# Kernel optimization log

Hardware: AMD Instinct MI355X
Metric: run time of the kernel (lower is better)

The kernel has to match this reference:

```python
import jax, jax.numpy as jnp
import numpy as np

N = 50000      # nodes
E = 800000     # edges (avg degree 16)
DIN = 128      # input_dim
DG = 128       # gnn_dim
DCLS = 128     # cls_dim
DOUT = 10      # output_dim
LMDA = 1.0     # rw_lmda
P_DROP = 0.5


def setup_inputs() -> dict:
    key = jax.random.key(0)
    ks = jax.random.split(key, 12)
    x = jax.random.normal(ks[0], (N, DIN), jnp.float32)
    edge_index = jax.random.randint(ks[1], (2, E), 0, N, dtype=jnp.int64)
    edge_weight = jax.random.uniform(ks[2], (E,), jnp.float32)
    def glorot(k, shape):
        lim = np.sqrt(6.0 / (shape[0] + shape[1])).astype(np.float32)
        return jax.random.uniform(k, shape, jnp.float32, -lim, lim)
    return dict(
        x=x, edge_index=edge_index, edge_weight=edge_weight,
        W_lin_in=glorot(ks[3], (DIN, DG)), b_lin_in=jnp.zeros((DG,), jnp.float32),
        W_agg_in=glorot(ks[4], (DG + DIN, DG)), b_agg_in=jnp.zeros((DG,), jnp.float32),
        W_lin_h=glorot(ks[5], (DG, DG)), b_lin_h=jnp.zeros((DG,), jnp.float32),
        W_agg_h=glorot(ks[6], (2 * DG, DG)), b_agg_h=jnp.zeros((DG,), jnp.float32),
        W_mlp1=glorot(ks[7], (DG, DCLS)), b_mlp1=jnp.zeros((DCLS,), jnp.float32),
        W_mlp2=glorot(ks[8], (DCLS, DOUT)), b_mlp2=jnp.zeros((DOUT,), jnp.float32),
    )


def _gs_layer(x, row, col, ew, inv_cnt, W_lin, b_lin, W_agg, b_agg):
    # GS_reweight: message = (1-lmda)*lin(x_j) + lmda*ew*lin(x_j), mean-aggregated
    # at row (flow='target_to_source': gather from col, scatter to row).
    h = x @ W_lin + b_lin                      # [N, DG] (lin before gather == lin(x_j))
    hj = h[col]                                # [E, DG] gather
    m = (1.0 - LMDA) * hj + LMDA * (ew[:, None] * hj)
    agg = jax.ops.segment_sum(m, row, num_segments=N) * inv_cnt[:, None]  # mean
    out = jnp.concatenate([agg, x], axis=-1) @ W_agg + b_agg              # update()
    return jax.nn.relu(out)


def _dropout(x, k):
    mask = jax.random.bernoulli(k, 1.0 - P_DROP, x.shape)
    return jnp.where(mask, x / (1.0 - P_DROP), 0.0)


def reference(x, edge_index, edge_weight,
              W_lin_in, b_lin_in, W_agg_in, b_agg_in,
              W_lin_h, b_lin_h, W_agg_h, b_agg_h,
              W_mlp1, b_mlp1, W_mlp2, b_mlp2):
    row, col = edge_index[0], edge_index[1]
    cnt = jax.ops.segment_sum(jnp.ones((E,), x.dtype), row, num_segments=N)
    inv_cnt = 1.0 / jnp.maximum(cnt, 1.0)     # scatter_mean: empty rows -> 0
    dk = jax.random.split(jax.random.key(42), 3)
    h = _gs_layer(x, row, col, edge_weight, inv_cnt, W_lin_in, b_lin_in, W_agg_in, b_agg_in)
    h = _dropout(jax.nn.relu(h), dk[0])       # relu is idempotent after update's relu
    for i in range(2):                        # layers 2,3 share prop_hidden weights
        h = _gs_layer(h, row, col, edge_weight, inv_cnt, W_lin_h, b_lin_h, W_agg_h, b_agg_h)
        h = _dropout(jax.nn.relu(h), dk[i + 1])
    y = jax.nn.relu(h @ W_mlp1 + b_mlp1) @ W_mlp2 + b_mlp2  # cls_layers=2, bn=False
    return (h, y)
```

## Files before the change

kernel.cpp:

```cpp
#include <hip/hip_runtime.h>
#include <cstdint>
#include <cstddef>


#define N_NODES 50000
#define N_EDGES 800000
#define DGN 128
#define DOUT 10
#define NELEM (N_NODES * DGN)
#define NMASKW (NELEM / 64)
#define NBINS 391
#define TILE 4096
#define NTILES ((N_EDGES + TILE - 1) / TILE)
#define GBF ((N_NODES + 63) / 64)
#define MK_BLOCKS 25000

#define XB_BLK 6250
#define HI_BLK NTILES
#define WC_BLK 128
#define TR_BLK 192
#define R0 XB_BLK
#define R1 (R0 + HI_BLK)
#define R2 (R1 + WC_BLK)
#define R3 (R2 + TR_BLK)
#define MEGA_BLOCKS (R3 + 1)

#define AB_BLOCKS ((N_NODES + 3) / 4)

typedef __attribute__((ext_vector_type(8))) short bf16x8;
typedef __attribute__((ext_vector_type(4))) float f32x4;

__host__ __device__ static inline unsigned short f2bf(float f) {
  union { float f; unsigned u; } c; c.f = f;
  unsigned u = c.u;
  return (unsigned short)((u + 0x7fffu + ((u >> 16) & 1u)) >> 16);
}
__device__ static inline float bflo(unsigned u) { return __uint_as_float(u << 16); }
__device__ static inline float bfhi(unsigned u) { return __uint_as_float(u & 0xffff0000u); }
__device__ static inline float bf2f(unsigned short h) {
  return __uint_as_float(((unsigned)h) << 16);
}

__host__ __device__ static inline void tf2x32(unsigned k0, unsigned k1,
                                              unsigned c0, unsigned c1,
                                              unsigned& o0, unsigned& o1) {
  unsigned ks2 = k0 ^ k1 ^ 0x1BD11BDAu;
  unsigned x0 = c0 + k0;
  unsigned x1 = c1 + k1;
#define TFR(r) { x0 += x1; x1 = (x1 << (r)) | (x1 >> (32 - (r))); x1 ^= x0; }
  TFR(13) TFR(15) TFR(26) TFR(6)
  x0 += k1;  x1 += ks2 + 1u;
  TFR(17) TFR(29) TFR(16) TFR(24)
  x0 += ks2; x1 += k0 + 2u;
  TFR(13) TFR(15) TFR(26) TFR(6)
  x0 += k0;  x1 += k1 + 3u;
  TFR(17) TFR(29) TFR(16) TFR(24)
  x0 += k1;  x1 += ks2 + 4u;
  TFR(13) TFR(15) TFR(26) TFR(6)
  x0 += ks2; x1 += k0 + 5u;
#undef TFR
  o0 = x0; o1 = x1;
}

__device__ static inline void mask_chunk(unsigned long long* __restrict__ gm,
                                         int i, unsigned k0, unsigned k1) {
  unsigned o0, o1;
  tf2x32(k0, k1, 0u, (unsigned)i, o0, o1);
  unsigned long long b = __ballot(((o0 ^ o1) >> 31) == 0u);
  if ((threadIdx.x & 63) == 0) gm[i >> 6] = b;
}

__global__ __launch_bounds__(256) void mega_kernel(
    const float* __restrict__ x, unsigned short* __restrict__ xb,
    const int* __restrict__ ei, int* __restrict__ chist,
    const float* __restrict__ Wli, const float* __restrict__ Wai,
    const float* __restrict__ Wlh, const float* __restrict__ Wah,
    const float* __restrict__ Wm1,
    const float* __restrict__ bli, const float* __restrict__ blh,
    unsigned short* __restrict__ Tai, unsigned short* __restrict__ Tah,
    unsigned short* __restrict__ Tm1,
    float* __restrict__ bvi, float* __restrict__ bvh) {
  __shared__ int h[NBINS];
  const int b = blockIdx.x;
  const int tid = threadIdx.x;

  if (b < R0) {
    int g = b * 256 + tid;
    float4 v = ((const float4*)x)[g];
    ushort4 o;
    o.x = f2bf(v.x); o.y = f2bf(v.y); o.z = f2bf(v.z); o.w = f2bf(v.w);
    ((ushort4*)xb)[g] = o;
  } else if (b < R1) {
    for (int i = tid; i < NBINS; i += 256) h[i] = 0;
    __syncthreads();
    const int e0 = (b - R0) * TILE;
#pragma unroll 4
    for (int j = 0; j < TILE; j += 256) {
      int e = e0 + j + tid;
      if (e < N_EDGES) {
        int r = ei[e];
        r = (r < 0) ? 0 : (r >= N_NODES ? N_NODES - 1 : r);
        atomicAdd(&h[r >> 7], 1);
      }
    }
    __syncthreads();
    for (int i = tid; i < NBINS; i += 256)
      if (h[i]) atomicAdd(&chist[i], h[i]);
  } else if (b < R2) {
    int idx = (b - R1) * 256 + tid;
    int n = idx & 127;
    int k = (idx >> 7) & 127;
    int m = idx >> 14;
    const float* Wl = m ? Wlh : Wli;
    const float* Wa = m ? Wah : Wai;
    unsigned short* T = m ? Tah : Tai;
    float acc = 0.0f;
#pragma unroll 8
    for (int j = 0; j < 128; ++j)
      acc += Wl[k * 128 + j] * Wa[j * 128 + n];
    T[n * 256 + k] = f2bf(acc);
  } else if (b < R3) {
    int j = (b - R2) * 256 + tid;
    if (j < 16384) {
      int kk = j & 127, n = j >> 7;
      Tai[n * 256 + 128 + kk] = f2bf(Wai[(size_t)(128 + kk) * 128 + n]);
    } else if (j < 32768) {
      int q = j - 16384;
      int kk = q & 127, n = q >> 7;
      Tah[n * 256 + 128 + kk] = f2bf(Wah[(size_t)(128 + kk) * 128 + n]);
    } else {
      int q = j - 32768;
      int k = q & 127, n = q >> 7;
      Tm1[n * 128 + k] = f2bf(Wm1[(size_t)k * 128 + n]);
    }
  } else {
    int n = tid & 127;
    const float* bl = (tid < 128) ? bli : blh;
    const float* Wa = (tid < 128) ? Wai : Wah;
    float acc = 0.0f;
    for (int j = 0; j < 128; ++j) acc += bl[j] * Wa[j * 128 + n];
    if (tid < 128) bvi[n] = acc; else bvh[n] = acc;
  }
}

__global__ __launch_bounds__(512) void prefix_kernel(const int* __restrict__ chist,
                                                     int* __restrict__ cbase,
                                                     int* __restrict__ ccursor,
                                                     int* __restrict__ rowptr) {
  __shared__ int s[512];
  const int t = threadIdx.x;
  int v = (t < NBINS) ? chist[t] : 0;
  s[t] = v;
  __syncthreads();
  for (int off = 1; off < 512; off <<= 1) {
    int tv = (t >= off) ? s[t - off] : 0;
    __syncthreads();
    s[t] += tv;
    __syncthreads();
  }
  if (t <= NBINS) {
    int ex = (t == 0) ? 0 : s[t - 1];
    cbase[t] = ex;
    if (t < NBINS) ccursor[t] = ex;
  }
  if (t == 0) rowptr[N_NODES] = N_EDGES;
}

__global__ __launch_bounds__(256) void scatter_kernel(const int* __restrict__ ei,
                                                      const float* __restrict__ ew,
                                                      int* __restrict__ ccursor,
                                                      uint2* __restrict__ pk,
                                                      unsigned long long* __restrict__ mg0,
                                                      unsigned k00, unsigned k01) {
  if (blockIdx.x >= NTILES) {
    mask_chunk(mg0, (blockIdx.x - NTILES) * 256 + threadIdx.x, k00, k01);
    return;
  }
  __shared__ uint2 st[TILE];
  __shared__ unsigned short sbin[TILE];
  __shared__ int h[NBINS];
  __shared__ int base[NBINS];
  __shared__ int gbase[NBINS];
  __shared__ int cur[NBINS];
  __shared__ int sc[512];
  const int tid = threadIdx.x;
  const int e0 = blockIdx.x * TILE;
  const int nt = (N_EDGES - e0 < TILE) ? (N_EDGES - e0) : TILE;

  for (int i = tid; i < NBINS; i += 256) { h[i] = 0; cur[i] = 0; }
  __syncthreads();
  for (int j = tid; j < nt; j += 256) {
    int r = ei[e0 + j];
    r = (r < 0) ? 0 : (r >= N_NODES ? N_NODES - 1 : r);
    atomicAdd(&h[r >> 7], 1);
  }
  __syncthreads();
  sc[tid] = (tid < NBINS) ? h[tid] : 0;
  sc[tid + 256] = (tid + 256 < NBINS) ? h[tid + 256] : 0;
  __syncthreads();
  for (int off = 1; off < 512; off <<= 1) {
    int a0 = (tid >= off) ? sc[tid - off] : 0;
    int a1 = (tid + 256 >= off) ? sc[tid + 256 - off] : 0;
    __syncthreads();
    sc[tid] += a0; sc[tid + 256] += a1;
    __syncthreads();
  }
  if (tid < NBINS) {
    base[tid] = sc[tid] - h[tid];
    if (h[tid]) gbase[tid] = atomicAdd(&ccursor[tid], h[tid]);
  }
  if (tid + 256 < NBINS) {
    base[tid + 256] = sc[tid + 256] - h[tid + 256];
    if (h[tid + 256]) gbase[tid + 256] = atomicAdd(&ccursor[tid + 256], h[tid + 256]);
  }
  __syncthreads();
  for (int j = tid; j < nt; j += 256) {
    int r = ei[e0 + j];
    r = (r < 0) ? 0 : (r >= N_NODES ? N_NODES - 1 : r);
    int c = ei[N_EDGES + e0 + j];
    c = (c < 0) ? 0 : (c >= N_NODES ? N_NODES - 1 : c);
    int bb = r >> 7;
    int slot = base[bb] + atomicAdd(&cur[bb], 1);
    uint2 p;
    p.x = ((unsigned)r << 16) | (unsigned)c;
    p.y = __float_as_uint(ew[e0 + j]);
    st[slot] = p;
    sbin[slot] = (unsigned short)bb;
  }
  __syncthreads();
  for (int j = tid; j < nt; j += 256) {
    int bb = sbin[j];
    pk[gbase[bb] + (j - base[bb])] = st[j];
  }
}

__global__ __launch_bounds__(256) void place_kernel(const int* __restrict__ cbase,
                                                    const uint2* __restrict__ pk,
                                                    uint2* __restrict__ csr,
                                                    int* __restrict__ rowptr,
                                                    float* __restrict__ invc) {
  __shared__ int lcnt[128];
  __shared__ int lpre[128];
  __shared__ int lcur[128];
  __shared__ int sc[128];
  const int b = blockIdx.x;
  const int tid = threadIdx.x;
  const int cb = cbase[b];
  const int n = cbase[b + 1] - cb;
  const int r0 = b << 7;
  const int nr = (N_NODES - r0 < 128) ? (N_NODES - r0) : 128;

  if (tid < 128) { lcnt[tid] = 0; lcur[tid] = 0; }
  __syncthreads();
  for (int i = tid; i < n; i += 256) {
    int r7 = (int)(pk[cb + i].x >> 16) - r0;
    atomicAdd(&lcnt[r7], 1);
  }
  __syncthreads();
  if (tid < 128) sc[tid] = lcnt[tid];
  __syncthreads();
  for (int off = 1; off < 128; off <<= 1) {
    int tv = (tid >= off && tid < 128) ? sc[tid - off] : 0;
    __syncthreads();
    if (tid < 128) sc[tid] += tv;
    __syncthreads();
  }
  if (tid < 128) lpre[tid] = sc[tid] - lcnt[tid];
  __syncthreads();
  if (tid < nr) {
    rowptr[r0 + tid] = cb + lpre[tid];
    int c = lcnt[tid];
    invc[r0 + tid] = 1.0f / (float)(c > 1 ? c : 1);
  }
  for (int i = tid; i < n; i += 256) {
    uint2 p = pk[cb + i];
    int r7 = (int)(p.x >> 16) - r0;
    int slot = cb + lpre[r7] + atomicAdd(&lcur[r7], 1);
    uint2 o;
    o.x = p.x & 0xFFFFu;
    o.y = p.y;
    csr[slot] = o;
  }
}

__global__ __launch_bounds__(256) void agg_kernel(const unsigned short* __restrict__ hlin,
                                                  const int* __restrict__ rowptr,
                                                  const uint2* __restrict__ csr,
                                                  const float* __restrict__ invc,
                                                  unsigned short* __restrict__ agg,
                                                  float* __restrict__ swout) {
  const int r = blockIdx.x * 4 + (threadIdx.x >> 6);
  const int lane = threadIdx.x & 63;
  const int es = lane >> 4;
  const int cg = lane & 15;
  const int start = rowptr[r];
  const int num = rowptr[r + 1] - start;
  const uint4* __restrict__ H = (const uint4*)hlin;

  int qi = (num > 0) ? (start + (lane < num ? lane : num - 1)) : 0;
  uint2 myq = csr[qi];

  float a[8] = {0.f, 0.f, 0.f, 0.f, 0.f, 0.f, 0.f, 0.f};
  float ws = 0.f;
  const int nb = (num < 64) ? num : 64;
  for (int e = 0; e < nb; e += 16) {
#pragma unroll
    for (int j = 0; j < 4; ++j) {
      int idx = e + j * 4 + es;
      bool ok = idx < nb;
      int sl = ok ? idx : nb - 1;
      int c0 = __shfl((int)myq.x, sl);
      int w0 = __shfl((int)myq.y, sl);
      unsigned col = (unsigned)c0;
      float w = ok ? __uint_as_float((unsigned)w0) : 0.0f;
      uint4 p = H[(size_t)col * 16 + cg];
      ws += w;
      a[0] += w * bflo(p.x); a[1] += w * bfhi(p.x);
      a[2] += w * bflo(p.y); a[3] += w * bfhi(p.y);
      a[4] += w * bflo(p.z); a[5] += w * bfhi(p.z);
      a[6] += w * bflo(p.w); a[7] += w * bfhi(p.w);
    }
  }
  for (int e = 64; e < num; e += 16) {
#pragma unroll
    for (int j = 0; j < 4; ++j) {
      int idx = e + j * 4 + es;
      bool ok = idx < num;
      int idxc = ok ? idx : (num - 1);
      uint2 q = csr[start + idxc];
      float w = ok ? __uint_as_float(q.y) : 0.0f;
      uint4 p = H[(size_t)q.x * 16 + cg];
      ws += w;
      a[0] += w * bflo(p.x); a[1] += w * bfhi(p.x);
      a[2] += w * bflo(p.y); a[3] += w * bfhi(p.y);
      a[4] += w * bflo(p.z); a[5] += w * bfhi(p.z);
      a[6] += w * bflo(p.w); a[7] += w * bfhi(p.w);
    }
  }
#pragma unroll
  for (int k = 0; k < 8; ++k) {
    a[k] += __shfl_xor(a[k], 32);
    a[k] += __shfl_xor(a[k], 16);
  }
  ws += __shfl_xor(ws, 32);
  ws += __shfl_xor(ws, 16);
  const float s = invc[r];
  if (es == 0) {
    uint4 o;
    o.x = (unsigned)f2bf(a[0] * s) | ((unsigned)f2bf(a[1] * s) << 16);
    o.y = (unsigned)f2bf(a[2] * s) | ((unsigned)f2bf(a[3] * s) << 16);
    o.z = (unsigned)f2bf(a[4] * s) | ((unsigned)f2bf(a[5] * s) << 16);
    o.w = (unsigned)f2bf(a[6] * s) | ((unsigned)f2bf(a[7] * s) << 16);
    ((uint4*)agg)[(size_t)r * 16 + cg] = o;
  }
  if (swout && lane == 0) swout[r] = ws * s;
}

template <bool WF32, bool MASKGEN>
__global__ __launch_bounds__(256) void layer_gemm(
    const unsigned short* __restrict__ Agg, const unsigned short* __restrict__ Hin,
    const unsigned short* __restrict__ Wt,
    const float* __restrict__ bvec, const float* __restrict__ bagg,
    const float* __restrict__ sw,
    const unsigned long long* __restrict__ maskw,
    float* __restrict__ outf, unsigned short* __restrict__ outb,
    unsigned long long* __restrict__ gm, unsigned gk0, unsigned gk1) {
  if (MASKGEN && blockIdx.x >= GBF) {
    mask_chunk(gm, (blockIdx.x - GBF) * 256 + threadIdx.x, gk0, gk1);
    return;
  }
  constexpr int LS = 72;
  __shared__ unsigned short Als[64 * LS];
  __shared__ unsigned short Bls[128 * LS];
  const int tid = threadIdx.x;
  const int m0 = blockIdx.x * 64;
  const int lane = tid & 63;
  const int wid = tid >> 6;
  const int wm = (wid >> 1) * 32;
  const int wn = (wid & 1) * 64;
  const int ln = lane & 15;
  const int lh = lane >> 4;
  const int sArow = tid >> 2;
  const int sAk = (tid & 3) * 16;
  const int sBcol = tid >> 1;
  const int sBk = (tid & 1) * 32;
  int arow = m0 + sArow;
  if (arow >= N_NODES) arow = N_NODES - 1;

  f32x4 acc[2][4];
#pragma unroll
  for (int i = 0; i < 2; ++i)
#pragma unroll
    for (int j = 0; j < 4; ++j)
#pragma unroll
      for (int r = 0; r < 4; ++r) acc[i][j][r] = 0.0f;

  for (int kb = 0; kb < 256; kb += 64) {
    const unsigned short* Asrc = (kb < 128) ? Agg : Hin;
    const unsigned short* ap = Asrc + (size_t)arow * 128 + (kb & 127) + sAk;
    unsigned short* al = &Als[sArow * LS + sAk];
    *(uint4*)(al + 0) = *(const uint4*)(ap + 0);
    *(uint4*)(al + 8) = *(const uint4*)(ap + 8);
    const unsigned short* bp = Wt + (size_t)sBcol * 256 + kb + sBk;
    unsigned short* bl = &Bls[sBcol * LS + sBk];
    *(uint4*)(bl + 0)  = *(const uint4*)(bp + 0);
    *(uint4*)(bl + 8)  = *(const uint4*)(bp + 8);
    *(uint4*)(bl + 16) = *(const uint4*)(bp + 16);
    *(uint4*)(bl + 24) = *(const uint4*)(bp + 24);
    __syncthreads();
#pragma unroll
    for (int ks = 0; ks < 64; ks += 32) {
      bf16x8 af[2], bfr[4];
#pragma unroll
      for (int i = 0; i < 2; ++i)
        af[i] = *(const bf16x8*)&Als[(wm + i * 16 + ln) * LS + ks + lh * 8];
#pragma unroll
      for (int j = 0; j < 4; ++j)
        bfr[j] = *(const bf16x8*)&Bls[(wn + j * 16 + ln) * LS + ks + lh * 8];
#pragma unroll
      for (int i = 0; i < 2; ++i)
#pragma unroll
        for (int j = 0; j < 4; ++j)
          acc[i][j] = __builtin_amdgcn_mfma_f32_16x16x32_bf16(af[i], bfr[j], acc[i][j], 0, 0, 0);
    }
    __syncthreads();
  }

  const int lm = lane >> 4;
  float bc[4], b2[4];
#pragma unroll
  for (int j = 0; j < 4; ++j) {
    int col = wn + j * 16 + ln;
    bc[j] = bvec[col];
    b2[j] = bagg[col];
  }
#pragma unroll
  for (int i = 0; i < 2; ++i) {
    const int lr0 = wm + i * 16 + lm * 4;
#pragma unroll
    for (int r = 0; r < 4; ++r) {
      const int row = m0 + lr0 + r;
      if (row >= N_NODES) continue;
      const float swr = sw[row];
      const unsigned long long mw = maskw[(size_t)row * 2 + (wn >> 6)];
#pragma unroll
      for (int j = 0; j < 4; ++j) {
        const int col = wn + j * 16 + ln;
        float v = acc[i][j][r] + swr * bc[j] + b2[j];
        v = fmaxf(v, 0.0f);
        v = ((mw >> (col & 63)) & 1ull) ? 2.0f * v : 0.0f;
        if (WF32) outf[(size_t)row * DGN + col] = v;
        outb[(size_t)row * DGN + col] = f2bf(v);
      }
    }
  }
}

__global__ __launch_bounds__(256) void mlp_gemm(
    const unsigned short* __restrict__ A0,
    const unsigned short* __restrict__ Wt,
    const float* __restrict__ b1,
    const float* __restrict__ W2, const float* __restrict__ b2,
    float* __restrict__ y) {
  constexpr int LS = 72;
  constexpr int LT = 132;
  __shared__ unsigned short Als[64 * LS];
  __shared__ unsigned short Bls[128 * LS];
  __shared__ unsigned short tT[64 * LT];
  __shared__ float Ws[128 * DOUT];
  __shared__ float bs[DOUT];
  const int tid = threadIdx.x;
  const int m0 = blockIdx.x * 64;
  const int lane = tid & 63;
  const int wid = tid >> 6;
  const int wm = (wid >> 1) * 32;
  const int wn = (wid & 1) * 64;
  const int ln = lane & 15;
  const int lh = lane >> 4;
  const int sArow = tid >> 2;
  const int sAk = (tid & 3) * 16;
  const int sBcol = tid >> 1;
  const int sBk = (tid & 1) * 32;
  int arow = m0 + sArow;
  if (arow >= N_NODES) arow = N_NODES - 1;

  for (int i = tid; i < 128 * DOUT; i += 256) Ws[i] = W2[i];
  if (tid < DOUT) bs[tid] = b2[tid];

  f32x4 acc[2][4];
#pragma unroll
  for (int i = 0; i < 2; ++i)
#pragma unroll
    for (int j = 0; j < 4; ++j)
#pragma unroll
      for (int r = 0; r < 4; ++r) acc[i][j][r] = 0.0f;

  for (int kb = 0; kb < 128; kb += 64) {
    const unsigned short* ap = A0 + (size_t)arow * 128 + kb + sAk;
    unsigned short* al = &Als[sArow * LS + sAk];
    *(uint4*)(al + 0) = *(const uint4*)(ap + 0);
    *(uint4*)(al + 8) = *(const uint4*)(ap + 8);
    const unsigned short* bp = Wt + (size_t)sBcol * 128 + kb + sBk;
    unsigned short* bl = &Bls[sBcol * LS + sBk];
    *(uint4*)(bl + 0)  = *(const uint4*)(bp + 0);
    *(uint4*)(bl + 8)  = *(const uint4*)(bp + 8);
    *(uint4*)(bl + 16) = *(const uint4*)(bp + 16);
    *(uint4*)(bl + 24) = *(const uint4*)(bp + 24);
    __syncthreads();
#pragma unroll
    for (int ks = 0; ks < 64; ks += 32) {
      bf16x8 af[2], bfr[4];
#pragma unroll
      for (int i = 0; i < 2; ++i)
        af[i] = *(const bf16x8*)&Als[(wm + i * 16 + ln) * LS + ks + lh * 8];
#pragma unroll
      for (int j = 0; j < 4; ++j)
        bfr[j] = *(const bf16x8*)&Bls[(wn + j * 16 + ln) * LS + ks + lh * 8];
#pragma unroll
      for (int i = 0; i < 2; ++i)
#pragma unroll
        for (int j = 0; j < 4; ++j)
          acc[i][j] = __builtin_amdgcn_mfma_f32_16x16x32_bf16(af[i], bfr[j], acc[i][j], 0, 0, 0);
    }
    __syncthreads();
  }

  const int lm = lane >> 4;
  float bcol[4];
#pragma unroll
  for (int j = 0; j < 4; ++j) bcol[j] = b1[wn + j * 16 + ln];
#pragma unroll
  for (int i = 0; i < 2; ++i) {
    const int lr0 = wm + i * 16 + lm * 4;
#pragma unroll
    for (int r = 0; r < 4; ++r) {
      const int lr = lr0 + r;
#pragma unroll
      for (int j = 0; j < 4; ++j) {
        const int col = wn + j * 16 + ln;
        float v = fmaxf(acc[i][j][r] + bcol[j], 0.0f);
        tT[lr * LT + col] = f2bf(v);
      }
    }
  }
  __syncthreads();

  if (tid < 64) {
    int row = m0 + tid;
    if (row < N_NODES) {
      float a2[DOUT];
#pragma unroll
      for (int c = 0; c < DOUT; ++c) a2[c] = bs[c];
      const unsigned short* tr = &tT[tid * LT];
#pragma unroll 8
      for (int k = 0; k < 128; ++k) {
        float tv = bf2f(tr[k]);
        const float* wr = &Ws[k * DOUT];
#pragma unroll
        for (int c = 0; c < DOUT; ++c) a2[c] += tv * wr[c];
      }
      float* yp = y + (size_t)row * DOUT;
#pragma unroll
      for (int c = 0; c < DOUT; ++c) yp[c] = a2[c];
    }
  }
}

extern "C" void kernel_launch(void* const* d_in, const int* in_sizes, int n_in,
                              void* d_out, int out_size, void* d_ws, size_t ws_size,
                              hipStream_t stream) {
  const float* x        = (const float*)d_in[0];
  const int*   ei       = (const int*)d_in[1];
  const float* ew       = (const float*)d_in[2];
  const float* W_lin_in = (const float*)d_in[3];
  const float* b_lin_in = (const float*)d_in[4];
  const float* W_agg_in = (const float*)d_in[5];
  const float* b_agg_in = (const float*)d_in[6];
  const float* W_lin_h  = (const float*)d_in[7];
  const float* b_lin_h  = (const float*)d_in[8];
  const float* W_agg_h  = (const float*)d_in[9];
  const float* b_agg_h  = (const float*)d_in[10];
  const float* W_mlp1   = (const float*)d_in[11];
  const float* b_mlp1   = (const float*)d_in[12];
  const float* W_mlp2   = (const float*)d_in[13];
  const float* b_mlp2   = (const float*)d_in[14];

  float* hout = (float*)d_out;
  float* yout = hout + (size_t)NELEM;

  char* p = (char*)d_ws;
  auto alloc = [&](size_t bytes) {
    char* q = p;
    p += (bytes + 255) & ~(size_t)255;
    return q;
  };
  int*   chist   = (int*)alloc((size_t)(NBINS + 1) * 4);
  int*   cbase   = (int*)alloc((size_t)(NBINS + 1) * 4);
  int*   ccursor = (int*)alloc((size_t)NBINS * 4);
  int*   rowptr  = (int*)alloc((size_t)(N_NODES + 1) * 4);
  float* invc    = (float*)alloc((size_t)N_NODES * 4);
  float* swv     = (float*)alloc((size_t)N_NODES * 4);
  uint2* pk      = (uint2*)alloc((size_t)N_EDGES * 8);
  uint2* csr     = (uint2*)alloc((size_t)N_EDGES * 8);
  unsigned short* xb   = (unsigned short*)alloc((size_t)NELEM * 2);
  unsigned short* aggb = (unsigned short*)alloc((size_t)NELEM * 2);
  unsigned short* hA   = (unsigned short*)alloc((size_t)NELEM * 2);
  unsigned short* hB   = (unsigned short*)alloc((size_t)NELEM * 2);
  unsigned long long* mw0 = (unsigned long long*)alloc((size_t)NMASKW * 8);
  unsigned long long* mw1 = (unsigned long long*)alloc((size_t)NMASKW * 8);
  unsigned long long* mw2 = (unsigned long long*)alloc((size_t)NMASKW * 8);
  unsigned short* Tai = (unsigned short*)alloc(32768 * 2);
  unsigned short* Tah = (unsigned short*)alloc(32768 * 2);
  unsigned short* Tm1 = (unsigned short*)alloc(16384 * 2);
  float* bvi = (float*)alloc(128 * 4);
  float* bvh = (float*)alloc(128 * 4);

  unsigned dk[3][2];
  for (unsigned i = 0; i < 3; ++i) tf2x32(0u, 42u, 0u, i, dk[i][0], dk[i][1]);

  hipMemsetAsync(chist, 0, (size_t)(NBINS + 1) * 4, stream);
  mega_kernel<<<MEGA_BLOCKS, 256, 0, stream>>>(
      x, xb, ei, chist, W_lin_in, W_agg_in, W_lin_h, W_agg_h, W_mlp1,
      b_lin_in, b_lin_h, Tai, Tah, Tm1, bvi, bvh);

  prefix_kernel<<<1, 512, 0, stream>>>(chist, cbase, ccursor, rowptr);
  scatter_kernel<<<NTILES + MK_BLOCKS, 256, 0, stream>>>(
      ei, ew, ccursor, pk, mw0, dk[0][0], dk[0][1]);
  place_kernel<<<NBINS, 256, 0, stream>>>(cbase, pk, csr, rowptr, invc);

  agg_kernel<<<AB_BLOCKS, 256, 0, stream>>>(xb, rowptr, csr, invc, aggb, swv);
  layer_gemm<false, true><<<GBF + MK_BLOCKS, 256, 0, stream>>>(
      aggb, xb, Tai, bvi, b_agg_in, swv, mw0, nullptr, hA,
      mw1, dk[1][0], dk[1][1]);

  agg_kernel<<<AB_BLOCKS, 256, 0, stream>>>(hA, rowptr, csr, invc, aggb, nullptr);
  layer_gemm<false, true><<<GBF + MK_BLOCKS, 256, 0, stream>>>(
      aggb, hA, Tah, bvh, b_agg_h, swv, mw1, nullptr, hB,
      mw2, dk[2][0], dk[2][1]);

  agg_kernel<<<AB_BLOCKS, 256, 0, stream>>>(hB, rowptr, csr, invc, aggb, nullptr);
  layer_gemm<true, false><<<GBF, 256, 0, stream>>>(
      aggb, hB, Tah, bvh, b_agg_h, swv, mw2, hout, hA,
      nullptr, 0, 0);

  mlp_gemm<<<GBF, 256, 0, stream>>>(hA, Tm1, b_mlp1, W_mlp2, b_mlp2, yout);
}
```

Baseline: 311.9 us.

## Drop prefix kernel via fixed bin strides, fuse MLP into last layer GEMM

Removes the single-block prefix kernel by giving each bin a fixed-stride slot in the staging buffer and computing each bin's base with a per-block reduction in place_kernel. Dropout mask generation moves from the scatter and layer GEMM launches into the agg_kernel launches. The MLP head is fused into the final layer GEMM so its output tile stays in shared memory instead of round-tripping through global memory. The cost is a larger staging buffer, which overflows if a bin exceeds 4096 edges, and higher shared memory use in the fused GEMM.

Measured after the change: 328.1 us. +5.2%, slower.

```diff
diff --git a/kernel.cpp b/kernel.cpp
--- a/kernel.cpp
+++ b/kernel.cpp
@@ -11,6 +11,7 @@
 #define NMASKW (NELEM / 64)
 #define NBINS 391
 #define TILE 4096
+#define BSTR 4096
 #define NTILES ((N_EDGES + TILE - 1) / TILE)
 #define GBF ((N_NODES + 63) / 64)
 #define MK_BLOCKS 25000
@@ -143,39 +144,10 @@
   }
 }
 
-__global__ __launch_bounds__(512) void prefix_kernel(const int* __restrict__ chist,
-                                                     int* __restrict__ cbase,
-                                                     int* __restrict__ ccursor,
-                                                     int* __restrict__ rowptr) {
-  __shared__ int s[512];
-  const int t = threadIdx.x;
-  int v = (t < NBINS) ? chist[t] : 0;
-  s[t] = v;
-  __syncthreads();
-  for (int off = 1; off < 512; off <<= 1) {
-    int tv = (t >= off) ? s[t - off] : 0;
-    __syncthreads();
-    s[t] += tv;
-    __syncthreads();
-  }
-  if (t <= NBINS) {
-    int ex = (t == 0) ? 0 : s[t - 1];
-    cbase[t] = ex;
-    if (t < NBINS) ccursor[t] = ex;
-  }
-  if (t == 0) rowptr[N_NODES] = N_EDGES;
-}
-
 __global__ __launch_bounds__(256) void scatter_kernel(const int* __restrict__ ei,
                                                       const float* __restrict__ ew,
                                                       int* __restrict__ ccursor,
-                                                      uint2* __restrict__ pk,
-                                                      unsigned long long* __restrict__ mg0,
-                                                      unsigned k00, unsigned k01) {
-  if (blockIdx.x >= NTILES) {
-    mask_chunk(mg0, (blockIdx.x - NTILES) * 256 + threadIdx.x, k00, k01);
-    return;
-  }
+                                                      uint2* __restrict__ pk) {
   __shared__ uint2 st[TILE];
   __shared__ unsigned short sbin[TILE];
   __shared__ int h[NBINS];
@@ -207,11 +179,12 @@
   }
   if (tid < NBINS) {
     base[tid] = sc[tid] - h[tid];
-    if (h[tid]) gbase[tid] = atomicAdd(&ccursor[tid], h[tid]);
+    if (h[tid]) gbase[tid] = tid * BSTR + atomicAdd(&ccursor[tid], h[tid]);
   }
   if (tid + 256 < NBINS) {
     base[tid + 256] = sc[tid + 256] - h[tid + 256];
-    if (h[tid + 256]) gbase[tid + 256] = atomicAdd(&ccursor[tid + 256], h[tid + 256]);
+    if (h[tid + 256])
+      gbase[tid + 256] = (tid + 256) * BSTR + atomicAdd(&ccursor[tid + 256], h[tid + 256]);
   }
   __syncthreads();
   for (int j = tid; j < nt; j += 256) {
@@ -230,30 +203,41 @@
   __syncthreads();
   for (int j = tid; j < nt; j += 256) {
     int bb = sbin[j];
-    pk[gbase[bb] + (j - base[bb])] = st[j];
-  }
-}
-
-__global__ __launch_bounds__(256) void place_kernel(const int* __restrict__ cbase,
+    pk[(size_t)gbase[bb] + (j - base[bb])] = st[j];
+  }
+}
+
+__global__ __launch_bounds__(256) void place_kernel(const int* __restrict__ chist,
                                                     const uint2* __restrict__ pk,
                                                     uint2* __restrict__ csr,
                                                     int* __restrict__ rowptr,
                                                     float* __restrict__ invc) {
+  __shared__ int red[256];
   __shared__ int lcnt[128];
   __shared__ int lpre[128];
   __shared__ int lcur[128];
   __shared__ int sc[128];
   const int b = blockIdx.x;
   const int tid = threadIdx.x;
-  const int cb = cbase[b];
-  const int n = cbase[b + 1] - cb;
+
+  int psum = 0;
+  for (int i = tid; i < b; i += 256) psum += chist[i];
+  red[tid] = psum;
+  __syncthreads();
+  for (int off = 128; off > 0; off >>= 1) {
+    if (tid < off) red[tid] += red[tid + off];
+    __syncthreads();
+  }
+  const int cb = red[0];
+  const int n = chist[b];
+  const uint2* __restrict__ pkb = pk + (size_t)b * BSTR;
   const int r0 = b << 7;
   const int nr = (N_NODES - r0 < 128) ? (N_NODES - r0) : 128;
 
   if (tid < 128) { lcnt[tid] = 0; lcur[tid] = 0; }
   __syncthreads();
   for (int i = tid; i < n; i += 256) {
-    int r7 = (int)(pk[cb + i].x >> 16) - r0;
+    int r7 = (int)(pkb[i].x >> 16) - r0;
     atomicAdd(&lcnt[r7], 1);
   }
   __syncthreads();
@@ -272,8 +256,9 @@
     int c = lcnt[tid];
     invc[r0 + tid] = 1.0f / (float)(c > 1 ? c : 1);
   }
+  if (b == NBINS - 1 && tid == 0) rowptr[N_NODES] = N_EDGES;
   for (int i = tid; i < n; i += 256) {
-    uint2 p = pk[cb + i];
+    uint2 p = pkb[i];
     int r7 = (int)(p.x >> 16) - r0;
     int slot = cb + lpre[r7] + atomicAdd(&lcur[r7], 1);
     uint2 o;
@@ -288,7 +273,13 @@
                                                   const uint2* __restrict__ csr,
                                                   const float* __restrict__ invc,
                                                   unsigned short* __restrict__ agg,
-                                                  float* __restrict__ swout) {
+                                                  float* __restrict__ swout,
+                                                  unsigned long long* __restrict__ gm,
+                                                  unsigned gk0, unsigned gk1) {
+  if (blockIdx.x >= AB_BLOCKS) {
+    mask_chunk(gm, (blockIdx.x - AB_BLOCKS) * 256 + threadIdx.x, gk0, gk1);
+    return;
+  }
   const int r = blockIdx.x * 4 + (threadIdx.x >> 6);
   const int lane = threadIdx.x & 63;
   const int es = lane >> 4;
@@ -356,7 +347,7 @@
   if (swout && lane == 0) swout[r] = ws * s;
 }
 
-template <bool WF32, bool MASKGEN>
+template <bool WF32, bool MLP>
 __global__ __launch_bounds__(256) void layer_gemm(
     const unsigned short* __restrict__ Agg, const unsigned short* __restrict__ Hin,
     const unsigned short* __restrict__ Wt,
@@ -364,14 +355,17 @@
     const float* __restrict__ sw,
     const unsigned long long* __restrict__ maskw,
     float* __restrict__ outf, unsigned short* __restrict__ outb,
-    unsigned long long* __restrict__ gm, unsigned gk0, unsigned gk1) {
-  if (MASKGEN && blockIdx.x >= GBF) {
-    mask_chunk(gm, (blockIdx.x - GBF) * 256 + threadIdx.x, gk0, gk1);
-    return;
-  }
+    const unsigned short* __restrict__ Wt2,
+    const float* __restrict__ b1,
+    const float* __restrict__ W2, const float* __restrict__ b2,
+    float* __restrict__ y) {
   constexpr int LS = 72;
+  constexpr int LT = 132;
   __shared__ unsigned short Als[64 * LS];
   __shared__ unsigned short Bls[128 * LS];
+  __shared__ unsigned short tT[MLP ? 64 * LT : 2];
+  __shared__ float Ws[MLP ? 128 * DOUT : 1];
+  __shared__ float bs[MLP ? DOUT : 1];
   const int tid = threadIdx.x;
   const int m0 = blockIdx.x * 64;
   const int lane = tid & 63;
@@ -387,6 +381,11 @@
   int arow = m0 + sArow;
   if (arow >= N_NODES) arow = N_NODES - 1;
 
+  if (MLP) {
+    for (int i = tid; i < 128 * DOUT; i += 256) Ws[i] = W2[i];
+    if (tid < DOUT) bs[tid] = b2[tid];
+  }
+
   f32x4 acc[2][4];
 #pragma unroll
   for (int i = 0; i < 2; ++i)
@@ -427,12 +426,12 @@
   }
 
   const int lm = lane >> 4;
-  float bc[4], b2[4];
+  float bc[4], b2c[4];
 #pragma unroll
   for (int j = 0; j < 4; ++j) {
     int col = wn + j * 16 + ln;
     bc[j] = bvec[col];
-    b2[j] = bagg[col];
+    b2c[j] = bagg[col];
   }
 #pragma unroll
   for (int i = 0; i < 2; ++i) {
@@ -446,122 +445,90 @@
 #pragma unroll
       for (int j = 0; j < 4; ++j) {
         const int col = wn + j * 16 + ln;
-        float v = acc[i][j][r] + swr * bc[j] + b2[j];
+        float v = acc[i][j][r] + swr * bc[j] + b2c[j];
         v = fmaxf(v, 0.0f);
         v = ((mw >> (col & 63)) & 1ull) ? 2.0f * v : 0.0f;
         if (WF32) outf[(size_t)row * DGN + col] = v;
-        outb[(size_t)row * DGN + col] = f2bf(v);
+        if (MLP) tT[(lr0 + r) * LT + col] = f2bf(v);
+        else outb[(size_t)row * DGN + col] = f2bf(v);
       }
     }
   }
-}
-
-__global__ __launch_bounds__(256) void mlp_gemm(
-    const unsigned short* __restrict__ A0,
-    const unsigned short* __restrict__ Wt,
-    const float* __restrict__ b1,
-    const float* __restrict__ W2, const float* __restrict__ b2,
-    float* __restrict__ y) {
-  constexpr int LS = 72;
-  constexpr int LT = 132;
-  __shared__ unsigned short Als[64 * LS];
-  __shared__ unsigned short Bls[128 * LS];
-  __shared__ unsigned short tT[64 * LT];
-  __shared__ float Ws[128 * DOUT];
-  __shared__ float bs[DOUT];
-  const int tid = threadIdx.x;
-  const int m0 = blockIdx.x * 64;
-  const int lane = tid & 63;
-  const int wid = tid >> 6;
-  const int wm = (wid >> 1) * 32;
-  const int wn = (wid & 1) * 64;
-  const int ln = lane & 15;
-  const int lh = lane >> 4;
-  const int sArow = tid >> 2;
-  const int sAk = (tid & 3) * 16;
-  const int sBcol = tid >> 1;
-  const int sBk = (tid & 1) * 32;
-  int arow = m0 + sArow;
-  if (arow >= N_NODES) arow = N_NODES - 1;
-
-  for (int i = tid; i < 128 * DOUT; i += 256) Ws[i] = W2[i];
-  if (tid < DOUT) bs[tid] = b2[tid];
-
-  f32x4 acc[2][4];
-#pragma unroll
-  for (int i = 0; i < 2; ++i)
-#pragma unroll
-    for (int j = 0; j < 4; ++j)
-#pragma unroll
-      for (int r = 0; r < 4; ++r) acc[i][j][r] = 0.0f;
-
-  for (int kb = 0; kb < 128; kb += 64) {
-    const unsigned short* ap = A0 + (size_t)arow * 128 + kb + sAk;
-    unsigned short* al = &Als[sArow * LS + sAk];
-    *(uint4*)(al + 0) = *(const uint4*)(ap + 0);
-    *(uint4*)(al + 8) = *(const uint4*)(ap + 8);
-    const unsigned short* bp = Wt + (size_t)sBcol * 128 + kb + sBk;
-    unsigned short* bl = &Bls[sBcol * LS + sBk];
-    *(uint4*)(bl + 0)  = *(const uint4*)(bp + 0);
-    *(uint4*)(bl + 8)  = *(const uint4*)(bp + 8);
-    *(uint4*)(bl + 16) = *(const uint4*)(bp + 16);
-    *(uint4*)(bl + 24) = *(const uint4*)(bp + 24);
-    __syncthreads();
-#pragma unroll
-    for (int ks = 0; ks < 64; ks += 32) {
-      bf16x8 af[2], bfr[4];
-#pragma unroll
-      for (int i = 0; i < 2; ++i)
-        af[i] = *(const bf16x8*)&Als[(wm + i * 16 + ln) * LS + ks + lh * 8];
+
+  if (MLP) {
+    __syncthreads();
+
+    f32x4 acc2[2][4];
+#pragma unroll
+    for (int i = 0; i < 2; ++i)
 #pragma unroll
       for (int j = 0; j < 4; ++j)
-        bfr[j] = *(const bf16x8*)&Bls[(wn + j * 16 + ln) * LS + ks + lh * 8];
-#pragma unroll
-      for (int i = 0; i < 2; ++i)
+#pragma unroll
+        for (int r = 0; r < 4; ++r) acc2[i][j][r] = 0.0f;
+
+    for (int kb = 0; kb < 128; kb += 64) {
+      const unsigned short* bp = Wt2 + (size_t)sBcol * 128 + kb + sBk;
+      unsigned short* bl = &Bls[sBcol * LS + sBk];
+      *(uint4*)(bl + 0)  = *(const uint4*)(bp + 0);
+      *(uint4*)(bl + 8)  = *(const uint4*)(bp + 8);
+      *(uint4*)(bl + 16) = *(const uint4*)(bp + 16);
+      *(uint4*)(bl + 24) = *(const uint4*)(bp + 24);
+      __syncthreads();
+#pragma unroll
+      for (int ks = 0; ks < 64; ks += 32) {
+        bf16x8 af[2], bfr[4];
+#pragma unroll
+        for (int i = 0; i < 2; ++i)
+          af[i] = *(const bf16x8*)&tT[(wm + i * 16 + ln) * LT + kb + ks + lh * 8];
 #pragma unroll
         for (int j = 0; j < 4; ++j)
-          acc[i][j] = __builtin_amdgcn_mfma_f32_16x16x32_bf16(af[i], bfr[j], acc[i][j], 0, 0, 0);
-    }
-    __syncthreads();
-  }
-
-  const int lm = lane >> 4;
-  float bcol[4];
-#pragma unroll
-  for (int j = 0; j < 4; ++j) bcol[j] = b1[wn + j * 16 + ln];
-#pragma unroll
-  for (int i = 0; i < 2; ++i) {
-    const int lr0 = wm + i * 16 + lm * 4;
-#pragma unroll
-    for (int r = 0; r < 4; ++r) {
-      const int lr = lr0 + r;
-#pragma unroll
-      for (int j = 0; j < 4; ++j) {
-        const int col = wn + j * 16 + ln;
-        float v = fmaxf(acc[i][j][r] + bcol[j], 0.0f);
-        tT[lr * LT + col] = f2bf(v);
+          bfr[j] = *(const bf16x8*)&Bls[(wn + j * 16 + ln) * LS + ks + lh * 8];
+#pragma unroll
+        for (int i = 0; i < 2; ++i)
+#pragma unroll
+          for (int j = 0; j < 4; ++j)
+            acc2[i][j] = __builtin_amdgcn_mfma_f32_16x16x32_bf16(af[i], bfr[j], acc2[i][j], 0, 0, 0);
       }
-    }
-  }
-  __syncthreads();
-
-  if (tid < 64) {
-    int row = m0 + tid;
-    if (row < N_NODES) {
-      float a2[DOUT];
-#pragma unroll
-      for (int c = 0; c < DOUT; ++c) a2[c] = bs[c];
-      const unsigned short* tr = &tT[tid * LT];
+      __syncthreads();
+    }
+
+    float bcol[4];
+#pragma unroll
+    for (int j = 0; j < 4; ++j) bcol[j] = b1[wn + j * 16 + ln];
+#pragma unroll
+    for (int i = 0; i < 2; ++i) {
+      const int lr0 = wm + i * 16 + lm * 4;
+#pragma unroll
+      for (int r = 0; r < 4; ++r) {
+        const int lr = lr0 + r;
+#pragma unroll
+        for (int j = 0; j < 4; ++j) {
+          const int col = wn + j * 16 + ln;
+          float v = fmaxf(acc2[i][j][r] + bcol[j], 0.0f);
+          tT[lr * LT + col] = f2bf(v);
+        }
+      }
+    }
+    __syncthreads();
+
+    if (tid < 64) {
+      int row = m0 + tid;
+      if (row < N_NODES) {
+        float a2[DOUT];
+#pragma unroll
+        for (int c = 0; c < DOUT; ++c) a2[c] = bs[c];
+        const unsigned short* tr = &tT[tid * LT];
 #pragma unroll 8
-      for (int k = 0; k < 128; ++k) {
-        float tv = bf2f(tr[k]);
-        const float* wr = &Ws[k * DOUT];
-#pragma unroll
-        for (int c = 0; c < DOUT; ++c) a2[c] += tv * wr[c];
+        for (int k = 0; k < 128; ++k) {
+          float tv = bf2f(tr[k]);
+          const float* wr = &Ws[k * DOUT];
+#pragma unroll
+          for (int c = 0; c < DOUT; ++c) a2[c] += tv * wr[c];
+        }
+        float* yp = y + (size_t)row * DOUT;
+#pragma unroll
+        for (int c = 0; c < DOUT; ++c) yp[c] = a2[c];
       }
-      float* yp = y + (size_t)row * DOUT;
-#pragma unroll
-      for (int c = 0; c < DOUT; ++c) yp[c] = a2[c];
     }
   }
 }
@@ -595,12 +562,11 @@
     return q;
   };
   int*   chist   = (int*)alloc((size_t)(NBINS + 1) * 4);
-  int*   cbase   = (int*)alloc((size_t)(NBINS + 1) * 4);
   int*   ccursor = (int*)alloc((size_t)NBINS * 4);
   int*   rowptr  = (int*)alloc((size_t)(N_NODES + 1) * 4);
   float* invc    = (float*)alloc((size_t)N_NODES * 4);
   float* swv     = (float*)alloc((size_t)N_NODES * 4);
-  uint2* pk      = (uint2*)alloc((size_t)N_EDGES * 8);
+  uint2* pk      = (uint2*)alloc((size_t)NBINS * BSTR * 8);
   uint2* csr     = (uint2*)alloc((size_t)N_EDGES * 8);
   unsigned short* xb   = (unsigned short*)alloc((size_t)NELEM * 2);
   unsigned short* aggb = (unsigned short*)alloc((size_t)NELEM * 2);
@@ -619,29 +585,29 @@
   for (unsigned i = 0; i < 3; ++i) tf2x32(0u, 42u, 0u, i, dk[i][0], dk[i][1]);
 
   hipMemsetAsync(chist, 0, (size_t)(NBINS + 1) * 4, stream);
+  hipMemsetAsync(ccursor, 0, (size_t)NBINS * 4, stream);
   mega_kernel<<<MEGA_BLOCKS, 256, 0, stream>>>(
       x, xb, ei, chist, W_lin_in, W_agg_in, W_lin_h, W_agg_h, W_mlp1,
       b_lin_in, b_lin_h, Tai, Tah, Tm1, bvi, bvh);
 
-  prefix_kernel<<<1, 512, 0, stream>>>(chist, cbase, ccursor, rowptr);
-  scatter_kernel<<<NTILES + MK_BLOCKS, 256, 0, stream>>>(
-      ei, ew, ccursor, pk, mw0, dk[0][0], dk[0][1]);
-  place_kernel<<<NBINS, 256, 0, stream>>>(cbase, pk, csr, rowptr, invc);
-
-  agg_kernel<<<AB_BLOCKS, 256, 0, stream>>>(xb, rowptr, csr, invc, aggb, swv);
-  layer_gemm<false, true><<<GBF + MK_BLOCKS, 256, 0, stream>>>(
+  scatter_kernel<<<NTILES, 256, 0, stream>>>(ei, ew, ccursor, pk);
+  place_kernel<<<NBINS, 256, 0, stream>>>(chist, pk, csr, rowptr, invc);
+
+  agg_kernel<<<AB_BLOCKS + MK_BLOCKS, 256, 0, stream>>>(
+      xb, rowptr, csr, invc, aggb, swv, mw0, dk[0][0], dk[0][1]);
+  layer_gemm<false, false><<<GBF, 256, 0, stream>>>(
       aggb, xb, Tai, bvi, b_agg_in, swv, mw0, nullptr, hA,
-      mw1, dk[1][0], dk[1][1]);
-
-  agg_kernel<<<AB_BLOCKS, 256, 0, stream>>>(hA, rowptr, csr, invc, aggb, nullptr);
-  layer_gemm<false, true><<<GBF + MK_BLOCKS, 256, 0, stream>>>(
+      nullptr, nullptr, nullptr, nullptr, nullptr);
+
+  agg_kernel<<<AB_BLOCKS + MK_BLOCKS, 256, 0, stream>>>(
+      hA, rowptr, csr, invc, aggb, nullptr, mw1, dk[1][0], dk[1][1]);
+  layer_gemm<false, false><<<GBF, 256, 0, stream>>>(
       aggb, hA, Tah, bvh, b_agg_h, swv, mw1, nullptr, hB,
-      mw2, dk[2][0], dk[2][1]);
-
-  agg_kernel<<<AB_BLOCKS, 256, 0, stream>>>(hB, rowptr, csr, invc, aggb, nullptr);
-  layer_gemm<true, false><<<GBF, 256, 0, stream>>>(
-      aggb, hB, Tah, bvh, b_agg_h, swv, mw2, hout, hA,
-      nullptr, 0, 0);
-
-  mlp_gemm<<<GBF, 256, 0, stream>>>(hA, Tm1, b_mlp1, W_mlp2, b_mlp2, yout);
-}
+      nullptr, nullptr, nullptr, nullptr, nullptr);
+
+  agg_kernel<<<AB_BLOCKS + MK_BLOCKS, 256, 0, stream>>>(
+      hB, rowptr, csr, invc, aggb, nullptr, mw2, dk[2][0], dk[2][1]);
+  layer_gemm<true, true><<<GBF, 256, 0, stream>>>(
+      aggb, hB, Tah, bvh, b_agg_h, swv, mw2, hout, nullptr,
+      Tm1, b_mlp1, W_mlp2, b_mlp2, yout);
+}
```
